# Kernel tuning notes

Hardware: AMD Instinct MI355X
Metric: run time of the kernel (lower is better)

Reference implementation:

```python
import jax, jax.numpy as jnp
import numpy as np

N4, N3, N2, N1, K = 32768, 65536, 131072, 262144, 16
G = 512


def _w(key, fan_in, fan_out):
    return jax.random.normal(key, (fan_in, fan_out), dtype=jnp.float32) / np.sqrt(fan_in)


def setup_inputs() -> dict:
    key = jax.random.key(0)
    ks = jax.random.split(key, 24)

    def edges(k, n_coarse, n_fine):
        # each fine (output) point gathers from K random coarse (input) points
        src = jax.random.randint(k, (n_fine * K,), 0, n_coarse, dtype=jnp.int32)
        dst = jnp.repeat(jnp.arange(n_fine, dtype=jnp.int32), K)
        return src, dst

    src3, dst3 = edges(ks[0], N4, N3)
    src2, dst2 = edges(ks[1], N3, N2)
    src1, dst1 = edges(ks[2], N2, N1)

    def gidx(k, n):
        return jnp.sort(jax.random.randint(k, (n,), 0, G, dtype=jnp.int32))

    inp = {
        'z_mask': jax.random.normal(ks[3], (N4, 64), dtype=jnp.float32),
        'pos4': jax.random.normal(ks[4], (N4, 3), dtype=jnp.float32),
        'pos3': jax.random.normal(ks[5], (N3, 3), dtype=jnp.float32),
        'pos2': jax.random.normal(ks[6], (N2, 3), dtype=jnp.float32),
        'pos1': jax.random.normal(ks[7], (N1, 3), dtype=jnp.float32),
        'g4': gidx(ks[8], N4), 'g3': gidx(ks[9], N3),
        'g2': gidx(ks[10], N2), 'g1': gidx(ks[11], N1),
        # PointConv MLP params: Linear(c_in+3 -> c_mid), CELU, Linear(c_mid -> c_out), max-aggregate
        'w1a': _w(ks[12], 64 + 3, 64), 'b1a': jnp.zeros((64,), jnp.float32),
        'w1b': _w(ks[13], 64, 32), 'b1b': jnp.zeros((32,), jnp.float32),
        'w2a': _w(ks[14], 32 + 3, 16), 'b2a': jnp.zeros((16,), jnp.float32),
        'w2b': _w(ks[15], 16, 16), 'b2b': jnp.zeros((16,), jnp.float32),
        'w3a': _w(ks[16], 16 + 3, 8), 'b3a': jnp.zeros((8,), jnp.float32),
        'w3b': _w(ks[17], 8, 8), 'b3b': jnp.zeros((8,), jnp.float32),
        'wlin': _w(ks[18], 8, 1), 'blin': jnp.zeros((1,), jnp.float32),
        'src3': src3, 'dst3': dst3,
        'src2': src2, 'dst2': dst2,
        'src1': src1, 'dst1': dst1,
    }
    return inp


def point_conv(x_in, pos_in, pos_out, src, dst, w_a, b_a, w_b, b_b, n_out):
    # gather: per-edge neighbor features + relative positions
    rel = pos_in[src] - pos_out[dst]                      # [E, 3]
    feat = jnp.concatenate([x_in[src], rel], axis=-1)     # [E, c_in+3]
    h = jax.nn.celu(feat @ w_a + b_a)                     # [E, c_mid]
    m = h @ w_b + b_b                                     # [E, c_out]
    # scatter: max-aggregate edge messages onto output points
    return jax.ops.segment_max(m, dst, num_segments=n_out)


def reference(z_mask, pos4, pos3, pos2, pos1, g4, g3, g2, g1,
              w1a, b1a, w1b, b1b, w2a, b2a, w2b, b2b, w3a, b3a, w3b, b3b,
              wlin, blin, src3, dst3, src2, dst2, src1, dst1):
    out = jax.nn.celu(point_conv(z_mask, pos4, pos3, src3, dst3, w1a, b1a, w1b, b1b, N3))
    out = jax.nn.celu(point_conv(out, pos3, pos2, src2, dst2, w2a, b2a, w2b, b2b, N2))
    out = jax.nn.celu(point_conv(out, pos2, pos1, src1, dst1, w3a, b3a, w3b, b3b, N1))
    logits = out @ wlin + blin                            # [N1, 1]
    return jax.nn.log_sigmoid(logits)
```

## Files before the change

kernel.cpp:

```cpp
#include <hip/hip_runtime.h>
#include <hip/hip_fp16.h>
#include <math.h>

#define N4C 32768
#define N3C 65536
#define N2C 131072
#define N1C 262144

typedef _Float16 f16x8 __attribute__((ext_vector_type(8)));
typedef float f32x4 __attribute__((ext_vector_type(4)));
typedef float f32x16 __attribute__((ext_vector_type(16)));

__device__ __forceinline__ f32x4 mfma16(f16x8 a, f16x8 b, f32x4 c) {
  return __builtin_amdgcn_mfma_f32_16x16x32_f16(a, b, c, 0, 0, 0);
}
__device__ __forceinline__ f32x16 mfma32(f16x8 a, f16x8 b, f32x16 c) {
  return __builtin_amdgcn_mfma_f32_32x32x16_f16(a, b, c, 0, 0, 0);
}

__device__ __forceinline__ float celuf(float x) {
  return fmaxf(x, 0.f) + (__expf(fminf(x, 0.f)) - 1.f);
}

__device__ __forceinline__ float logsigf(float x) {
  float e = __expf(-fabsf(x));
  return fminf(x, 0.f) - __logf(1.f + e);
}

__device__ __forceinline__ float max3f(float a, float b, float c) {
  return fmaxf(fmaxf(a, b), c);
}

__device__ __forceinline__ _Float16 exp2_16(_Float16 x) {
  __half h; __builtin_memcpy(&h, &x, 2);
  h = hexp2(h);
  _Float16 r; __builtin_memcpy(&r, &h, 2);
  return r;
}

__device__ __forceinline__ f16x8 celu8p1(f16x8 x) {
  f16x8 z = {};
  f16x8 mx = __builtin_elementwise_max(x, z);
  f16x8 mn = __builtin_elementwise_min(x, z) * (_Float16)1.44269504f;
#pragma unroll
  for (int i = 0; i < 8; ++i) mn[i] = exp2_16(mn[i]);
  return mx + mn;
}

__global__ __launch_bounds__(256) void y4_kernel(
    const float* __restrict__ z, const float* __restrict__ pos4,
    const float* __restrict__ pos3, const float* __restrict__ w1a,
    const float* __restrict__ b1a, _Float16* __restrict__ y4,
    _Float16* __restrict__ vt3) {
  if (blockIdx.x >= 512) {
    const int idx = (blockIdx.x - 512) * 256 + threadIdx.x;
    const int p = idx >> 3, seg = (idx & 7) * 8;
    const float q0 = pos3[p * 3 + 0];
    const float q1 = pos3[p * 3 + 1];
    const float q2 = pos3[p * 3 + 2];
    f16x8 v;
#pragma unroll
    for (int j = 0; j < 8; ++j) {
      const int k = seg + j;
      v[j] = (_Float16)(w1a[64 * 64 + k] * q0 + w1a[65 * 64 + k] * q1 +
                        w1a[66 * 64 + k] * q2);
    }
    *(f16x8*)(vt3 + (size_t)p * 64 + seg) = v;
    return;
  }
  const int lane = threadIdx.x & 63, wid = threadIdx.x >> 6;
  const int col = lane & 15, quad = lane >> 4;
  const int base = (blockIdx.x * 4 + wid) * 16;

  f16x8 Ba[2][4];
#pragma unroll
  for (int c = 0; c < 2; ++c)
#pragma unroll
    for (int t = 0; t < 4; ++t)
#pragma unroll
      for (int j = 0; j < 8; ++j)
        Ba[c][t][j] = (_Float16)w1a[(c * 32 + quad * 8 + j) * 64 + t * 16 + col];

  float wr[3][4];
#pragma unroll
  for (int c = 0; c < 3; ++c)
#pragma unroll
    for (int t = 0; t < 4; ++t)
      wr[c][t] = w1a[(64 + c) * 64 + t * 16 + col];

  float px[4], py[4], pz[4];
#pragma unroll
  for (int r = 0; r < 4; ++r) {
    const int row = base + quad * 4 + r;
    px[r] = pos4[row * 3 + 0];
    py[r] = pos4[row * 3 + 1];
    pz[r] = pos4[row * 3 + 2];
  }

  const float* zr = z + (size_t)(base + col) * 64;
  f16x8 A0, A1;
  {
    float4 f0 = *(const float4*)(zr + quad * 8);
    float4 f1 = *(const float4*)(zr + quad * 8 + 4);
    float4 f2 = *(const float4*)(zr + 32 + quad * 8);
    float4 f3 = *(const float4*)(zr + 32 + quad * 8 + 4);
    A0[0] = (_Float16)f0.x; A0[1] = (_Float16)f0.y; A0[2] = (_Float16)f0.z; A0[3] = (_Float16)f0.w;
    A0[4] = (_Float16)f1.x; A0[5] = (_Float16)f1.y; A0[6] = (_Float16)f1.z; A0[7] = (_Float16)f1.w;
    A1[0] = (_Float16)f2.x; A1[1] = (_Float16)f2.y; A1[2] = (_Float16)f2.z; A1[3] = (_Float16)f2.w;
    A1[4] = (_Float16)f3.x; A1[5] = (_Float16)f3.y; A1[6] = (_Float16)f3.z; A1[7] = (_Float16)f3.w;
  }
#pragma unroll
  for (int t = 0; t < 4; ++t) {
    f32x4 acc = {0.f, 0.f, 0.f, 0.f};
    acc = mfma16(A0, Ba[0][t], acc);
    acc = mfma16(A1, Ba[1][t], acc);
    const float bt = b1a[t * 16 + col];
#pragma unroll
    for (int r = 0; r < 4; ++r) {
      const float posterm =
          px[r] * wr[0][t] + py[r] * wr[1][t] + pz[r] * wr[2][t];
      y4[(size_t)(base + quad * 4 + r) * 64 + t * 16 + col] =
          (_Float16)(acc[r] + bt + posterm);
    }
  }
}

__global__ __launch_bounds__(256) void y3_kernel(
    const _Float16* __restrict__ x3f, const float* __restrict__ pos3,
    const float* __restrict__ pos2, const float* __restrict__ w2a,
    const float* __restrict__ b2a, _Float16* __restrict__ y3,
    _Float16* __restrict__ vt2) {
  if (blockIdx.x >= 1024) {
    const int idx = (blockIdx.x - 1024) * 256 + threadIdx.x;
    const int p = idx >> 1, seg = (idx & 1) * 8;
    const float q0 = pos2[p * 3 + 0];
    const float q1 = pos2[p * 3 + 1];
    const float q2 = pos2[p * 3 + 2];
    f16x8 v;
#pragma unroll
    for (int j = 0; j < 8; ++j) {
      const int k = seg + j;
      v[j] = (_Float16)(w2a[32 * 16 + k] * q0 + w2a[33 * 16 + k] * q1 +
                        w2a[34 * 16 + k] * q2);
    }
    *(f16x8*)(vt2 + (size_t)p * 16 + seg) = v;
    return;
  }
  const int lane = threadIdx.x & 63, wid = threadIdx.x >> 6;
  const int col = lane & 15, quad = lane >> 4;
  const int base = (blockIdx.x * 4 + wid) * 16;

  f16x8 B;
#pragma unroll
  for (int j = 0; j < 8; ++j) B[j] = (_Float16)w2a[(quad * 8 + j) * 16 + col];

  float wr[3];
#pragma unroll
  for (int c = 0; c < 3; ++c) wr[c] = w2a[(32 + c) * 16 + col];

  float px[4], py[4], pz[4];
#pragma unroll
  for (int r = 0; r < 4; ++r) {
    const int row = base + quad * 4 + r;
    px[r] = pos3[row * 3 + 0];
    py[r] = pos3[row * 3 + 1];
    pz[r] = pos3[row * 3 + 2];
  }

  f16x8 A = *(const f16x8*)(x3f + (size_t)(base + col) * 32 + quad * 8);
  f32x4 d = {0.f, 0.f, 0.f, 0.f};
  d = mfma16(A, B, d);
  const float bt = b2a[col];
#pragma unroll
  for (int r = 0; r < 4; ++r) {
    const float posterm = px[r] * wr[0] + py[r] * wr[1] + pz[r] * wr[2];
    y3[(size_t)(base + quad * 4 + r) * 16 + col] =
        (_Float16)(d[r] + bt + posterm);
  }
}

__global__ __launch_bounds__(256) void y2_kernel(
    const _Float16* __restrict__ x2f, const float* __restrict__ pos2,
    const float* __restrict__ pos1, const float* __restrict__ w3a,
    const float* __restrict__ b3a, _Float16* __restrict__ y2,
    _Float16* __restrict__ vt1) {
  if (blockIdx.x >= 2048) {
    const int p = (blockIdx.x - 2048) * 256 + threadIdx.x;
    const float q0 = pos1[p * 3 + 0];
    const float q1 = pos1[p * 3 + 1];
    const float q2 = pos1[p * 3 + 2];
    f16x8 v;
#pragma unroll
    for (int k = 0; k < 8; ++k)
      v[k] = (_Float16)(w3a[16 * 8 + k] * q0 + w3a[17 * 8 + k] * q1 +
                        w3a[18 * 8 + k] * q2);
    *(f16x8*)(vt1 + (size_t)p * 8) = v;
    return;
  }
  const int lane = threadIdx.x & 63, wid = threadIdx.x >> 6;
  const int col = lane & 15, quad = lane >> 4;
  const int base = (blockIdx.x * 4 + wid) * 16;

  f16x8 B;
#pragma unroll
  for (int j = 0; j < 8; ++j) {
    int k = quad * 8 + j;
    B[j] = (k < 16 && col < 8) ? (_Float16)w3a[k * 8 + col] : (_Float16)0.f;
  }
  f16x8 A = *(const f16x8*)(x2f + (size_t)(base + col) * 16 + (quad & 1) * 8);
  f32x4 d = {0.f, 0.f, 0.f, 0.f};
  d = mfma16(A, B, d);
  if (col < 8) {
    float wr[3];
#pragma unroll
    for (int c = 0; c < 3; ++c) wr[c] = w3a[(16 + c) * 8 + col];
    const float bt = b3a[col];
#pragma unroll
    for (int r = 0; r < 4; ++r) {
      const int row = base + quad * 4 + r;
      const float posterm = pos2[row * 3 + 0] * wr[0] +
                            pos2[row * 3 + 1] * wr[1] +
                            pos2[row * 3 + 2] * wr[2];
      y2[(size_t)row * 8 + col] = (_Float16)(d[r] + bt + posterm);
    }
  }
}

__global__ __launch_bounds__(256) void l3_kernel(
    const _Float16* __restrict__ y4, const _Float16* __restrict__ vt3,
    const int* __restrict__ src3, const float* __restrict__ w1b,
    const float* __restrict__ b1b, _Float16* __restrict__ x3f) {
  const int lane = threadIdx.x & 63, wid = threadIdx.x >> 6;
  const int n = lane & 31;
  const int kh = lane >> 5;

  f16x8 Bb[4];
#pragma unroll
  for (int ks = 0; ks < 4; ++ks)
#pragma unroll
    for (int j = 0; j < 8; ++j)
      Bb[ks][j] = (_Float16)w1b[(ks * 16 + kh * 8 + j) * 32 + n];

  float s = 0.f;
#pragma unroll 4
  for (int k = 0; k < 32; ++k) s += w1b[(kh * 32 + k) * 32 + n];
  s += __shfl_xor(s, 32, 64);
  const float biasB = b1b[n] - s;

  const int gwave = blockIdx.x * 4 + wid;
  const int nw = gridDim.x << 2;

#pragma unroll 1
  for (int pb = gwave * 2; pb < N3C; pb += nw * 2) {
    const int s1 = src3[pb * 16 + n];
    const int p = pb + (n >> 4);
    const _Float16* yrow = y4 + (size_t)s1 * 64 + kh * 8;
    const _Float16* vrow = vt3 + (size_t)p * 64 + kh * 8;

    f16x8 A[4];
#pragma unroll
    for (int ks = 0; ks < 4; ++ks)
      A[ks] = *(const f16x8*)(yrow + ks * 16) - *(const f16x8*)(vrow + ks * 16);
#pragma unroll
    for (int ks = 0; ks < 4; ++ks) A[ks] = celu8p1(A[ks]);

    f32x16 acc = {};
#pragma unroll
    for (int ks = 0; ks < 4; ++ks) acc = mfma32(A[ks], Bb[ks], acc);

    float mA = fmaxf(max3f(max3f(acc[0], acc[1], acc[2]),
                           max3f(acc[3], acc[4], acc[5]), acc[6]), acc[7]);
    float mB = fmaxf(max3f(max3f(acc[8], acc[9], acc[10]),
                           max3f(acc[11], acc[12], acc[13]), acc[14]), acc[15]);
    mA = fmaxf(mA, __shfl_xor(mA, 32, 64));
    mB = fmaxf(mB, __shfl_xor(mB, 32, 64));

    const float mv = kh ? mB : mA;
    x3f[(size_t)(pb + kh) * 32 + n] = (_Float16)celuf(mv + biasB);
  }
}

__device__ __forceinline__ void l2_compute(
    int pr, f16x8 A_in, f16x8 vt, f16x8 Bb, float biasB, int kh, int n,
    _Float16* __restrict__ x2f) {
  f16x8 A = celu8p1(A_in - vt);
  f32x16 acc = {};
  acc = mfma32(A, Bb, acc);

  float mA = fmaxf(max3f(max3f(acc[0], acc[1], acc[2]),
                         max3f(acc[3], acc[4], acc[5]), acc[6]), acc[7]);
  float mB = fmaxf(max3f(max3f(acc[8], acc[9], acc[10]),
                         max3f(acc[11], acc[12], acc[13]), acc[14]), acc[15]);
  mA = fmaxf(mA, __shfl_xor(mA, 32, 64));
  mB = fmaxf(mB, __shfl_xor(mB, 32, 64));

  if (n < 16) {
    const float m = kh ? mB : mA;
    x2f[(size_t)(2 * pr + kh) * 16 + n] = (_Float16)celuf(m + biasB);
  }
}

__global__ __launch_bounds__(256) void l2_kernel(
    const _Float16* __restrict__ y3, const _Float16* __restrict__ vt2,
    const int* __restrict__ src2, const float* __restrict__ w2b,
    const float* __restrict__ b2b, _Float16* __restrict__ x2f) {
  const int lane = threadIdx.x & 63, wid = threadIdx.x >> 6;
  const int n = lane & 31;
  const int e = lane & 15;
  const int h = (lane >> 4) & 1;
  const int kh = lane >> 5;

  f16x8 Bb;
#pragma unroll
  for (int j = 0; j < 8; ++j)
    Bb[j] = (n < 16) ? (_Float16)w2b[(kh * 8 + j) * 16 + n] : (_Float16)0.f;
  float ws = 0.f;
#pragma unroll
  for (int k = 0; k < 16; ++k) ws += w2b[k * 16 + (n & 15)];
  const float biasB = b2b[n & 15] - ws;

  const int gwave = blockIdx.x * 4 + wid;
  const int nw = gridDim.x << 2;

#pragma unroll 1
  for (int pr = gwave; pr < N2C / 2; pr += 2 * nw) {
    const int pr2 = pr + nw;
    const int pa = 2 * pr + h, pb = 2 * pr2 + h;
    const int sa = src2[pa * 16 + e];
    const int sb = src2[pb * 16 + e];

    f16x8 Aa = *(const f16x8*)(y3 + (size_t)sa * 16 + kh * 8);
    f16x8 Ab = *(const f16x8*)(y3 + (size_t)sb * 16 + kh * 8);
    f16x8 va = *(const f16x8*)(vt2 + (size_t)pa * 16 + kh * 8);
    f16x8 vb = *(const f16x8*)(vt2 + (size_t)pb * 16 + kh * 8);

    l2_compute(pr,  Aa, va, Bb, biasB, kh, n, x2f);
    l2_compute(pr2, Ab, vb, Bb, biasB, kh, n, x2f);
  }
}

__device__ __forceinline__ void l1_compute(
    int pb, f16x8 A_in, f16x8 vt, f16x8 Bb, float biasB, float wl, float bl,
    int lane, float* __restrict__ out) {
  f16x8 A = celu8p1(A_in - vt);
  f32x16 acc = {};
  acc = mfma32(A, Bb, acc);

  float mA = fmaxf(max3f(max3f(acc[0], acc[1], acc[2]),
                         max3f(acc[3], acc[4], acc[5]), acc[6]), acc[7]);
  float mB = fmaxf(max3f(max3f(acc[8], acc[9], acc[10]),
                         max3f(acc[11], acc[12], acc[13]), acc[14]), acc[15]);
  mA = fmaxf(mA, __shfl_xor(mA, 32, 64));
  mB = fmaxf(mB, __shfl_xor(mB, 32, 64));

  float tA = celuf(mA + biasB) * wl;
  float tB = celuf(mB + biasB) * wl;
  tA += __shfl_xor(tA, 1, 64);
  tA += __shfl_xor(tA, 2, 64);
  tA += __shfl_xor(tA, 4, 64);
  tB += __shfl_xor(tB, 1, 64);
  tB += __shfl_xor(tB, 2, 64);
  tB += __shfl_xor(tB, 4, 64);
  if (lane == 0) {
    float2 o; o.x = logsigf(tA + bl); o.y = logsigf(tB + bl);
    *(float2*)(out + pb) = o;
  } else if (lane == 8) {
    float2 o; o.x = logsigf(tA + bl); o.y = logsigf(tB + bl);
    *(float2*)(out + pb + 2) = o;
  }
}

__global__ __launch_bounds__(256) void l1_kernel(
    const _Float16* __restrict__ y2, const _Float16* __restrict__ vt1,
    const int* __restrict__ src1, const float* __restrict__ w3b,
    const float* __restrict__ b3b, const float* __restrict__ wlin,
    const float* __restrict__ blin, float* __restrict__ out) {
  const int lane = threadIdx.x & 63, wid = threadIdx.x >> 6;
  const int m = lane & 31;
  const int e = lane & 15;
  const int h = (lane >> 4) & 1;
  const int kh = lane >> 5;
  const int g = 2 * kh + h;

  f16x8 Bb;
  const int n = m;
#pragma unroll
  for (int j = 0; j < 8; ++j)
    Bb[j] = (n < 16 && (n >> 3) == kh) ? (_Float16)w3b[j * 8 + (n & 7)]
                                       : (_Float16)0.f;
  float ws = 0.f;
#pragma unroll
  for (int j = 0; j < 8; ++j) ws += w3b[j * 8 + (n & 7)];
  const float biasB = (n < 16) ? b3b[n & 7] - ws : 0.f;
  const float wl = (n < 16) ? wlin[n & 7] : 0.f;
  const float bl = blin[0];

  const int gwave = blockIdx.x * 4 + wid;
  const int nw = gridDim.x << 2;

#pragma unroll 1
  for (int q = gwave; q < N1C / 4; q += 2 * nw) {
    const int q2 = q + nw;
    const int pba = q * 4, pbb = q2 * 4;
    const int pa = pba + g, pb = pbb + g;
    const int sa = src1[pa * 16 + e];
    const int sb = src1[pb * 16 + e];

    f16x8 Aa = *(const f16x8*)(y2 + (size_t)sa * 8);
    f16x8 Ab = *(const f16x8*)(y2 + (size_t)sb * 8);
    f16x8 va = *(const f16x8*)(vt1 + (size_t)pa * 8);
    f16x8 vb = *(const f16x8*)(vt1 + (size_t)pb * 8);

    l1_compute(pba, Aa, va, Bb, biasB, wl, bl, lane, out);
    l1_compute(pbb, Ab, vb, Bb, biasB, wl, bl, lane, out);
  }
}

extern "C" void kernel_launch(void* const* d_in, const int* in_sizes, int n_in,
                              void* d_out, int out_size, void* d_ws, size_t ws_size,
                              hipStream_t stream) {
  const float* z_mask = (const float*)d_in[0];
  const float* pos4 = (const float*)d_in[1];
  const float* pos3 = (const float*)d_in[2];
  const float* pos2 = (const float*)d_in[3];
  const float* pos1 = (const float*)d_in[4];
  const float* w1a = (const float*)d_in[9];
  const float* b1a = (const float*)d_in[10];
  const float* w1b = (const float*)d_in[11];
  const float* b1b = (const float*)d_in[12];
  const float* w2a = (const float*)d_in[13];
  const float* b2a = (const float*)d_in[14];
  const float* w2b = (const float*)d_in[15];
  const float* b2b = (const float*)d_in[16];
  const float* w3a = (const float*)d_in[17];
  const float* b3a = (const float*)d_in[18];
  const float* w3b = (const float*)d_in[19];
  const float* b3b = (const float*)d_in[20];
  const float* wlin = (const float*)d_in[21];
  const float* blin = (const float*)d_in[22];
  const int* src3 = (const int*)d_in[23];
  const int* src2 = (const int*)d_in[25];
  const int* src1 = (const int*)d_in[27];

  char* w = (char*)d_ws;
  _Float16* y4  = (_Float16*)(w);
  _Float16* vt3 = (_Float16*)(w + (4u << 20));
  _Float16* x3f = (_Float16*)(w + (12u << 20));
  _Float16* y3  = (_Float16*)(w);
  _Float16* vt2 = (_Float16*)(w + (4u << 20));
  _Float16* x2f = (_Float16*)(w + (8u << 20));
  _Float16* y2  = (_Float16*)(w + (2u << 20));
  _Float16* vt1 = (_Float16*)(w + (12u << 20));
  float* out = (float*)d_out;

  y4_kernel<<<2560, 256, 0, stream>>>(z_mask, pos4, pos3, w1a, b1a, y4, vt3);
  l3_kernel<<<2048, 256, 0, stream>>>(y4, vt3, src3, w1b, b1b, x3f);
  y3_kernel<<<2048, 256, 0, stream>>>(x3f, pos3, pos2, w2a, b2a, y3, vt2);
  l2_kernel<<<2048, 256, 0, stream>>>(y3, vt2, src2, w2b, b2b, x2f);
  y2_kernel<<<3072, 256, 0, stream>>>(x2f, pos2, pos1, w3a, b3a, y2, vt1);
  l1_kernel<<<2048, 256, 0, stream>>>(y2, vt1, src1, w3b, b3b,
                                      wlin, blin, out);
}
```

Measured before the change: 235.0 us.

## Software-pipeline edge index loads and deepen per-wave work in gather kernels

The three gather kernels now prefetch the next iteration's source indices before processing the current one, so the index-load latency overlaps the dependent feature gathers and MFMA work. L2 and L1 move from two to three points per iteration, with bounds guards. L3 uses a fixed four-iteration loop with a hardcoded stride of 8192 waves, which assumes a specific grid size. These changes raise register pressure and couple L3 correctness to the launch configuration.

```diff
diff --git a/kernel.cpp b/kernel.cpp
--- a/kernel.cpp
+++ b/kernel.cpp
@@ -226,6 +226,36 @@
   }
 }
 
+__device__ __forceinline__ void l3_body(
+    int pb, int s1, int kh, int n, const _Float16* __restrict__ y4,
+    const _Float16* __restrict__ vt3, const f16x8 Bb[4], float biasB,
+    _Float16* __restrict__ x3f) {
+  const int p = pb + (n >> 4);
+  const _Float16* yrow = y4 + (size_t)s1 * 64 + kh * 8;
+  const _Float16* vrow = vt3 + (size_t)p * 64 + kh * 8;
+
+  f16x8 A[4];
+#pragma unroll
+  for (int ks = 0; ks < 4; ++ks)
+    A[ks] = *(const f16x8*)(yrow + ks * 16) - *(const f16x8*)(vrow + ks * 16);
+#pragma unroll
+  for (int ks = 0; ks < 4; ++ks) A[ks] = celu8p1(A[ks]);
+
+  f32x16 acc = {};
+#pragma unroll
+  for (int ks = 0; ks < 4; ++ks) acc = mfma32(A[ks], Bb[ks], acc);
+
+  float mA = fmaxf(max3f(max3f(acc[0], acc[1], acc[2]),
+                         max3f(acc[3], acc[4], acc[5]), acc[6]), acc[7]);
+  float mB = fmaxf(max3f(max3f(acc[8], acc[9], acc[10]),
+                         max3f(acc[11], acc[12], acc[13]), acc[14]), acc[15]);
+  mA = fmaxf(mA, __shfl_xor(mA, 32, 64));
+  mB = fmaxf(mB, __shfl_xor(mB, 32, 64));
+
+  const float mv = kh ? mB : mA;
+  x3f[(size_t)(pb + kh) * 32 + n] = (_Float16)celuf(mv + biasB);
+}
+
 __global__ __launch_bounds__(256) void l3_kernel(
     const _Float16* __restrict__ y4, const _Float16* __restrict__ vt3,
     const int* __restrict__ src3, const float* __restrict__ w1b,
@@ -247,36 +277,15 @@
   s += __shfl_xor(s, 32, 64);
   const float biasB = b1b[n] - s;
 
-  const int gwave = blockIdx.x * 4 + wid;
-  const int nw = gridDim.x << 2;
-
+  const int gw = blockIdx.x * 4 + wid;
+
+  int sCur = src3[(2 * gw) * 16 + n];
 #pragma unroll 1
-  for (int pb = gwave * 2; pb < N3C; pb += nw * 2) {
-    const int s1 = src3[pb * 16 + n];
-    const int p = pb + (n >> 4);
-    const _Float16* yrow = y4 + (size_t)s1 * 64 + kh * 8;
-    const _Float16* vrow = vt3 + (size_t)p * 64 + kh * 8;
-
-    f16x8 A[4];
-#pragma unroll
-    for (int ks = 0; ks < 4; ++ks)
-      A[ks] = *(const f16x8*)(yrow + ks * 16) - *(const f16x8*)(vrow + ks * 16);
-#pragma unroll
-    for (int ks = 0; ks < 4; ++ks) A[ks] = celu8p1(A[ks]);
-
-    f32x16 acc = {};
-#pragma unroll
-    for (int ks = 0; ks < 4; ++ks) acc = mfma32(A[ks], Bb[ks], acc);
-
-    float mA = fmaxf(max3f(max3f(acc[0], acc[1], acc[2]),
-                           max3f(acc[3], acc[4], acc[5]), acc[6]), acc[7]);
-    float mB = fmaxf(max3f(max3f(acc[8], acc[9], acc[10]),
-                           max3f(acc[11], acc[12], acc[13]), acc[14]), acc[15]);
-    mA = fmaxf(mA, __shfl_xor(mA, 32, 64));
-    mB = fmaxf(mB, __shfl_xor(mB, 32, 64));
-
-    const float mv = kh ? mB : mA;
-    x3f[(size_t)(pb + kh) * 32 + n] = (_Float16)celuf(mv + biasB);
+  for (int k = 0; k < 4; ++k) {
+    const int kn = (k < 3) ? k + 1 : 3;
+    const int sNext = src3[(2 * (gw + kn * 8192)) * 16 + n];
+    l3_body(2 * (gw + k * 8192), sCur, kh, n, y4, vt3, Bb, biasB, x3f);
+    sCur = sNext;
   }
 }
 
@@ -321,21 +330,40 @@
 
   const int gwave = blockIdx.x * 4 + wid;
   const int nw = gridDim.x << 2;
+  const int lim = N2C / 2;
+
+  int sA = src2[(2 * gwave + h) * 16 + e];
+  int sB = src2[(2 * (gwave + nw) + h) * 16 + e];
+  int sC = src2[(2 * (gwave + 2 * nw) + h) * 16 + e];
 
 #pragma unroll 1
-  for (int pr = gwave; pr < N2C / 2; pr += 2 * nw) {
-    const int pr2 = pr + nw;
-    const int pa = 2 * pr + h, pb = 2 * pr2 + h;
-    const int sa = src2[pa * 16 + e];
-    const int sb = src2[pb * 16 + e];
-
-    f16x8 Aa = *(const f16x8*)(y3 + (size_t)sa * 16 + kh * 8);
-    f16x8 Ab = *(const f16x8*)(y3 + (size_t)sb * 16 + kh * 8);
-    f16x8 va = *(const f16x8*)(vt2 + (size_t)pa * 16 + kh * 8);
-    f16x8 vb = *(const f16x8*)(vt2 + (size_t)pb * 16 + kh * 8);
-
-    l2_compute(pr,  Aa, va, Bb, biasB, kh, n, x2f);
-    l2_compute(pr2, Ab, vb, Bb, biasB, kh, n, x2f);
+  for (int base = gwave; base < lim; base += 3 * nw) {
+    const bool ok1 = base + nw < lim;
+    const bool ok2 = base + 2 * nw < lim;
+    const int pr1 = ok1 ? base + nw : base;
+    const int pr2 = ok2 ? base + 2 * nw : base;
+    const int pa0 = 2 * base + h, pa1 = 2 * pr1 + h, pa2 = 2 * pr2 + h;
+
+    f16x8 Aa = *(const f16x8*)(y3 + (size_t)sA * 16 + kh * 8);
+    f16x8 va = *(const f16x8*)(vt2 + (size_t)pa0 * 16 + kh * 8);
+    f16x8 Ab = *(const f16x8*)(y3 + (size_t)sB * 16 + kh * 8);
+    f16x8 vb = *(const f16x8*)(vt2 + (size_t)pa1 * 16 + kh * 8);
+    f16x8 Ac = *(const f16x8*)(y3 + (size_t)sC * 16 + kh * 8);
+    f16x8 vc = *(const f16x8*)(vt2 + (size_t)pa2 * 16 + kh * 8);
+
+    const int nb = base + 3 * nw;
+    const int n0 = nb < lim ? nb : base;
+    const int n1 = nb + nw < lim ? nb + nw : n0;
+    const int n2 = nb + 2 * nw < lim ? nb + 2 * nw : n0;
+    const int sAn = src2[(2 * n0 + h) * 16 + e];
+    const int sBn = src2[(2 * n1 + h) * 16 + e];
+    const int sCn = src2[(2 * n2 + h) * 16 + e];
+
+    l2_compute(base, Aa, va, Bb, biasB, kh, n, x2f);
+    if (ok1) l2_compute(base + nw, Ab, vb, Bb, biasB, kh, n, x2f);
+    if (ok2) l2_compute(base + 2 * nw, Ac, vc, Bb, biasB, kh, n, x2f);
+
+    sA = sAn; sB = sBn; sC = sCn;
   }
 }
 
@@ -377,10 +405,8 @@
     const float* __restrict__ blin, float* __restrict__ out) {
   const int lane = threadIdx.x & 63, wid = threadIdx.x >> 6;
   const int m = lane & 31;
-  const int e = lane & 15;
-  const int h = (lane >> 4) & 1;
   const int kh = lane >> 5;
-  const int g = 2 * kh + h;
+  const int g = 2 * kh + ((lane >> 4) & 1);
 
   f16x8 Bb;
   const int n = m;
@@ -397,22 +423,40 @@
 
   const int gwave = blockIdx.x * 4 + wid;
   const int nw = gridDim.x << 2;
+  const int lim = N1C / 4;
+
+  int sA = src1[gwave * 64 + lane];
+  int sB = src1[(gwave + nw) * 64 + lane];
+  int sC = src1[(gwave + 2 * nw) * 64 + lane];
 
 #pragma unroll 1
-  for (int q = gwave; q < N1C / 4; q += 2 * nw) {
-    const int q2 = q + nw;
-    const int pba = q * 4, pbb = q2 * 4;
-    const int pa = pba + g, pb = pbb + g;
-    const int sa = src1[pa * 16 + e];
-    const int sb = src1[pb * 16 + e];
-
-    f16x8 Aa = *(const f16x8*)(y2 + (size_t)sa * 8);
-    f16x8 Ab = *(const f16x8*)(y2 + (size_t)sb * 8);
-    f16x8 va = *(const f16x8*)(vt1 + (size_t)pa * 8);
-    f16x8 vb = *(const f16x8*)(vt1 + (size_t)pb * 8);
-
-    l1_compute(pba, Aa, va, Bb, biasB, wl, bl, lane, out);
-    l1_compute(pbb, Ab, vb, Bb, biasB, wl, bl, lane, out);
+  for (int base = gwave; base < lim; base += 3 * nw) {
+    const bool ok1 = base + nw < lim;
+    const bool ok2 = base + 2 * nw < lim;
+    const int q1 = ok1 ? base + nw : base;
+    const int q2 = ok2 ? base + 2 * nw : base;
+    const int p0 = base * 4 + g, p1 = q1 * 4 + g, p2 = q2 * 4 + g;
+
+    f16x8 Aa = *(const f16x8*)(y2 + (size_t)sA * 8);
+    f16x8 va = *(const f16x8*)(vt1 + (size_t)p0 * 8);
+    f16x8 Ab = *(const f16x8*)(y2 + (size_t)sB * 8);
+    f16x8 vb = *(const f16x8*)(vt1 + (size_t)p1 * 8);
+    f16x8 Ac = *(const f16x8*)(y2 + (size_t)sC * 8);
+    f16x8 vc = *(const f16x8*)(vt1 + (size_t)p2 * 8);
+
+    const int nb = base + 3 * nw;
+    const int m0 = nb < lim ? nb : base;
+    const int m1 = nb + nw < lim ? nb + nw : m0;
+    const int m2 = nb + 2 * nw < lim ? nb + 2 * nw : m0;
+    const int sAn = src1[m0 * 64 + lane];
+    const int sBn = src1[m1 * 64 + lane];
+    const int sCn = src1[m2 * 64 + lane];
+
+    l1_compute(base * 4, Aa, va, Bb, biasB, wl, bl, lane, out);
+    if (ok1) l1_compute((base + nw) * 4, Ab, vb, Bb, biasB, wl, bl, lane, out);
+    if (ok2) l1_compute((base + 2 * nw) * 4, Ac, vc, Bb, biasB, wl, bl, lane, out);
+
+    sA = sAn; sB = sBn; sC = sCn;
   }
 }
 
```

Result: slower. 242.1 us (+3.0%).

## Fuse five stage kernels into one cooperative persistent kernel with grid syncs

Applied to the files above, without the earlier changes.

Replaces the five separate launches after y4 with a single cooperative kernel of 1024 blocks that runs l3, y3, l2, y2 and l1 in sequence, separated by grid.sync(). If the cooperative launch fails it falls back to the separate kernels. The aim is to remove per-launch gaps and tail effects between small, dependent kernels. The cost is fewer blocks per stage, less latency hiding in the gather-heavy stages, and grid-barrier overhead. The l1 source-index load is also rewritten as one contiguous q*64+lane read.

```diff
diff --git a/kernel.cpp b/kernel.cpp
--- a/kernel.cpp
+++ b/kernel.cpp
@@ -1,6 +1,9 @@
 #include <hip/hip_runtime.h>
 #include <hip/hip_fp16.h>
+#include <hip/hip_cooperative_groups.h>
 #include <math.h>
+
+namespace cg = cooperative_groups;
 
 #define N4C 32768
 #define N3C 65536
@@ -125,6 +128,61 @@
   }
 }
 
+
+__global__ __launch_bounds__(256) void l3_kernel(
+    const _Float16* __restrict__ y4, const _Float16* __restrict__ vt3,
+    const int* __restrict__ src3, const float* __restrict__ w1b,
+    const float* __restrict__ b1b, _Float16* __restrict__ x3f) {
+  const int lane = threadIdx.x & 63, wid = threadIdx.x >> 6;
+  const int n = lane & 31;
+  const int kh = lane >> 5;
+
+  f16x8 Bb[4];
+#pragma unroll
+  for (int ks = 0; ks < 4; ++ks)
+#pragma unroll
+    for (int j = 0; j < 8; ++j)
+      Bb[ks][j] = (_Float16)w1b[(ks * 16 + kh * 8 + j) * 32 + n];
+
+  float s = 0.f;
+#pragma unroll 4
+  for (int k = 0; k < 32; ++k) s += w1b[(kh * 32 + k) * 32 + n];
+  s += __shfl_xor(s, 32, 64);
+  const float biasB = b1b[n] - s;
+
+  const int gwave = blockIdx.x * 4 + wid;
+  const int nw = gridDim.x << 2;
+
+#pragma unroll 1
+  for (int pb = gwave * 2; pb < N3C; pb += nw * 2) {
+    const int s1 = src3[pb * 16 + n];
+    const int p = pb + (n >> 4);
+    const _Float16* yrow = y4 + (size_t)s1 * 64 + kh * 8;
+    const _Float16* vrow = vt3 + (size_t)p * 64 + kh * 8;
+
+    f16x8 A[4];
+#pragma unroll
+    for (int ks = 0; ks < 4; ++ks)
+      A[ks] = *(const f16x8*)(yrow + ks * 16) - *(const f16x8*)(vrow + ks * 16);
+#pragma unroll
+    for (int ks = 0; ks < 4; ++ks) A[ks] = celu8p1(A[ks]);
+
+    f32x16 acc = {};
+#pragma unroll
+    for (int ks = 0; ks < 4; ++ks) acc = mfma32(A[ks], Bb[ks], acc);
+
+    float mA = fmaxf(max3f(max3f(acc[0], acc[1], acc[2]),
+                           max3f(acc[3], acc[4], acc[5]), acc[6]), acc[7]);
+    float mB = fmaxf(max3f(max3f(acc[8], acc[9], acc[10]),
+                           max3f(acc[11], acc[12], acc[13]), acc[14]), acc[15]);
+    mA = fmaxf(mA, __shfl_xor(mA, 32, 64));
+    mB = fmaxf(mB, __shfl_xor(mB, 32, 64));
+
+    const float mv = kh ? mB : mA;
+    x3f[(size_t)(pb + kh) * 32 + n] = (_Float16)celuf(mv + biasB);
+  }
+}
+
 __global__ __launch_bounds__(256) void y3_kernel(
     const _Float16* __restrict__ x3f, const float* __restrict__ pos3,
     const float* __restrict__ pos2, const float* __restrict__ w2a,
@@ -223,60 +281,6 @@
                             pos2[row * 3 + 2] * wr[2];
       y2[(size_t)row * 8 + col] = (_Float16)(d[r] + bt + posterm);
     }
-  }
-}
-
-__global__ __launch_bounds__(256) void l3_kernel(
-    const _Float16* __restrict__ y4, const _Float16* __restrict__ vt3,
-    const int* __restrict__ src3, const float* __restrict__ w1b,
-    const float* __restrict__ b1b, _Float16* __restrict__ x3f) {
-  const int lane = threadIdx.x & 63, wid = threadIdx.x >> 6;
-  const int n = lane & 31;
-  const int kh = lane >> 5;
-
-  f16x8 Bb[4];
-#pragma unroll
-  for (int ks = 0; ks < 4; ++ks)
-#pragma unroll
-    for (int j = 0; j < 8; ++j)
-      Bb[ks][j] = (_Float16)w1b[(ks * 16 + kh * 8 + j) * 32 + n];
-
-  float s = 0.f;
-#pragma unroll 4
-  for (int k = 0; k < 32; ++k) s += w1b[(kh * 32 + k) * 32 + n];
-  s += __shfl_xor(s, 32, 64);
-  const float biasB = b1b[n] - s;
-
-  const int gwave = blockIdx.x * 4 + wid;
-  const int nw = gridDim.x << 2;
-
-#pragma unroll 1
-  for (int pb = gwave * 2; pb < N3C; pb += nw * 2) {
-    const int s1 = src3[pb * 16 + n];
-    const int p = pb + (n >> 4);
-    const _Float16* yrow = y4 + (size_t)s1 * 64 + kh * 8;
-    const _Float16* vrow = vt3 + (size_t)p * 64 + kh * 8;
-
-    f16x8 A[4];
-#pragma unroll
-    for (int ks = 0; ks < 4; ++ks)
-      A[ks] = *(const f16x8*)(yrow + ks * 16) - *(const f16x8*)(vrow + ks * 16);
-#pragma unroll
-    for (int ks = 0; ks < 4; ++ks) A[ks] = celu8p1(A[ks]);
-
-    f32x16 acc = {};
-#pragma unroll
-    for (int ks = 0; ks < 4; ++ks) acc = mfma32(A[ks], Bb[ks], acc);
-
-    float mA = fmaxf(max3f(max3f(acc[0], acc[1], acc[2]),
-                           max3f(acc[3], acc[4], acc[5]), acc[6]), acc[7]);
-    float mB = fmaxf(max3f(max3f(acc[8], acc[9], acc[10]),
-                           max3f(acc[11], acc[12], acc[13]), acc[14]), acc[15]);
-    mA = fmaxf(mA, __shfl_xor(mA, 32, 64));
-    mB = fmaxf(mB, __shfl_xor(mB, 32, 64));
-
-    const float mv = kh ? mB : mA;
-    x3f[(size_t)(pb + kh) * 32 + n] = (_Float16)celuf(mv + biasB);
   }
 }
 
@@ -377,10 +381,8 @@
     const float* __restrict__ blin, float* __restrict__ out) {
   const int lane = threadIdx.x & 63, wid = threadIdx.x >> 6;
   const int m = lane & 31;
-  const int e = lane & 15;
-  const int h = (lane >> 4) & 1;
   const int kh = lane >> 5;
-  const int g = 2 * kh + h;
+  const int g = 2 * kh + ((lane >> 4) & 1);
 
   f16x8 Bb;
   const int n = m;
@@ -403,8 +405,8 @@
     const int q2 = q + nw;
     const int pba = q * 4, pbb = q2 * 4;
     const int pa = pba + g, pb = pbb + g;
-    const int sa = src1[pa * 16 + e];
-    const int sb = src1[pb * 16 + e];
+    const int sa = src1[q * 64 + lane];
+    const int sb = src1[q2 * 64 + lane];
 
     f16x8 Aa = *(const f16x8*)(y2 + (size_t)sa * 8);
     f16x8 Ab = *(const f16x8*)(y2 + (size_t)sb * 8);
@@ -413,6 +415,237 @@
 
     l1_compute(pba, Aa, va, Bb, biasB, wl, bl, lane, out);
     l1_compute(pbb, Ab, vb, Bb, biasB, wl, bl, lane, out);
+  }
+}
+
+struct FArgs {
+  const _Float16* y4; const _Float16* vt3; const int* src3;
+  const float* w1b; const float* b1b; _Float16* x3f;
+  const float* pos3; const float* pos2; const float* w2a; const float* b2a;
+  _Float16* y3; _Float16* vt2;
+  const int* src2; const float* w2b; const float* b2b; _Float16* x2f;
+  const float* pos1; const float* w3a; const float* b3a;
+  _Float16* y2; _Float16* vt1;
+  const int* src1; const float* w3b; const float* b3b;
+  const float* wlin; const float* blin; float* out;
+};
+
+__global__ __launch_bounds__(256, 4) void fused_kernel(FArgs a) {
+  const cg::grid_group grid = cg::this_grid();
+  const int lane = threadIdx.x & 63, wid = threadIdx.x >> 6;
+  const int blk = blockIdx.x;
+  const int gwave = blk * 4 + wid;
+  const int nw = gridDim.x << 2;
+
+  {
+    const int n = lane & 31;
+    const int kh = lane >> 5;
+
+    f16x8 Bb[4];
+#pragma unroll
+    for (int ks = 0; ks < 4; ++ks)
+#pragma unroll
+      for (int j = 0; j < 8; ++j)
+        Bb[ks][j] = (_Float16)a.w1b[(ks * 16 + kh * 8 + j) * 32 + n];
+
+    float s = 0.f;
+#pragma unroll 4
+    for (int k = 0; k < 32; ++k) s += a.w1b[(kh * 32 + k) * 32 + n];
+    s += __shfl_xor(s, 32, 64);
+    const float biasB = a.b1b[n] - s;
+
+#pragma unroll 1
+    for (int pb = gwave * 2; pb < N3C; pb += nw * 2) {
+      const int s1 = a.src3[pb * 16 + n];
+      const int p = pb + (n >> 4);
+      const _Float16* yrow = a.y4 + (size_t)s1 * 64 + kh * 8;
+      const _Float16* vrow = a.vt3 + (size_t)p * 64 + kh * 8;
+
+      f16x8 A[4];
+#pragma unroll
+      for (int ks = 0; ks < 4; ++ks)
+        A[ks] = *(const f16x8*)(yrow + ks * 16) - *(const f16x8*)(vrow + ks * 16);
+#pragma unroll
+      for (int ks = 0; ks < 4; ++ks) A[ks] = celu8p1(A[ks]);
+
+      f32x16 acc = {};
+#pragma unroll
+      for (int ks = 0; ks < 4; ++ks) acc = mfma32(A[ks], Bb[ks], acc);
+
+      float mA = fmaxf(max3f(max3f(acc[0], acc[1], acc[2]),
+                             max3f(acc[3], acc[4], acc[5]), acc[6]), acc[7]);
+      float mB = fmaxf(max3f(max3f(acc[8], acc[9], acc[10]),
+                             max3f(acc[11], acc[12], acc[13]), acc[14]), acc[15]);
+      mA = fmaxf(mA, __shfl_xor(mA, 32, 64));
+      mB = fmaxf(mB, __shfl_xor(mB, 32, 64));
+
+      const float mv = kh ? mB : mA;
+      a.x3f[(size_t)(pb + kh) * 32 + n] = (_Float16)celuf(mv + biasB);
+    }
+  }
+  grid.sync();
+
+  {
+    const int col = lane & 15, quad = lane >> 4;
+    const int base = gwave * 16;
+
+    f16x8 B;
+#pragma unroll
+    for (int j = 0; j < 8; ++j)
+      B[j] = (_Float16)a.w2a[(quad * 8 + j) * 16 + col];
+
+    float wr[3];
+#pragma unroll
+    for (int c = 0; c < 3; ++c) wr[c] = a.w2a[(32 + c) * 16 + col];
+
+    float px[4], py[4], pz[4];
+#pragma unroll
+    for (int r = 0; r < 4; ++r) {
+      const int row = base + quad * 4 + r;
+      px[r] = a.pos3[row * 3 + 0];
+      py[r] = a.pos3[row * 3 + 1];
+      pz[r] = a.pos3[row * 3 + 2];
+    }
+
+    f16x8 A = *(const f16x8*)(a.x3f + (size_t)(base + col) * 32 + quad * 8);
+    f32x4 d = {0.f, 0.f, 0.f, 0.f};
+    d = mfma16(A, B, d);
+    const float bt = a.b2a[col];
+#pragma unroll
+    for (int r = 0; r < 4; ++r) {
+      const float posterm = px[r] * wr[0] + py[r] * wr[1] + pz[r] * wr[2];
+      a.y3[(size_t)(base + quad * 4 + r) * 16 + col] =
+          (_Float16)(d[r] + bt + posterm);
+    }
+
+    const int idx = blk * 256 + threadIdx.x;
+    const int p = idx >> 1, seg = (idx & 1) * 8;
+    const float q0 = a.pos2[p * 3 + 0];
+    const float q1 = a.pos2[p * 3 + 1];
+    const float q2 = a.pos2[p * 3 + 2];
+    f16x8 v;
+#pragma unroll
+    for (int j = 0; j < 8; ++j) {
+      const int k = seg + j;
+      v[j] = (_Float16)(a.w2a[32 * 16 + k] * q0 + a.w2a[33 * 16 + k] * q1 +
+                        a.w2a[34 * 16 + k] * q2);
+    }
+    *(f16x8*)(a.vt2 + (size_t)p * 16 + seg) = v;
+  }
+  grid.sync();
+
+  {
+    const int n = lane & 31;
+    const int e = lane & 15;
+    const int h = (lane >> 4) & 1;
+    const int kh = lane >> 5;
+
+    f16x8 Bb;
+#pragma unroll
+    for (int j = 0; j < 8; ++j)
+      Bb[j] = (n < 16) ? (_Float16)a.w2b[(kh * 8 + j) * 16 + n] : (_Float16)0.f;
+    float ws = 0.f;
+#pragma unroll
+    for (int k = 0; k < 16; ++k) ws += a.w2b[k * 16 + (n & 15)];
+    const float biasB = a.b2b[n & 15] - ws;
+
+#pragma unroll 1
+    for (int pr = gwave; pr < N2C / 2; pr += 2 * nw) {
+      const int pr2 = pr + nw;
+      const int pa = 2 * pr + h, pb = 2 * pr2 + h;
+      const int sa = a.src2[pa * 16 + e];
+      const int sb = a.src2[pb * 16 + e];
+
+      f16x8 Aa = *(const f16x8*)(a.y3 + (size_t)sa * 16 + kh * 8);
+      f16x8 Ab = *(const f16x8*)(a.y3 + (size_t)sb * 16 + kh * 8);
+      f16x8 va = *(const f16x8*)(a.vt2 + (size_t)pa * 16 + kh * 8);
+      f16x8 vb = *(const f16x8*)(a.vt2 + (size_t)pb * 16 + kh * 8);
+
+      l2_compute(pr,  Aa, va, Bb, biasB, kh, n, a.x2f);
+      l2_compute(pr2, Ab, vb, Bb, biasB, kh, n, a.x2f);
+    }
+  }
+  grid.sync();
+
+  {
+    const int col = lane & 15, quad = lane >> 4;
+#pragma unroll 1
+    for (int b2 = blk; b2 < 2048; b2 += 1024) {
+      const int base = (b2 * 4 + wid) * 16;
+
+      f16x8 B;
+#pragma unroll
+      for (int j = 0; j < 8; ++j) {
+        int k = quad * 8 + j;
+        B[j] = (k < 16 && col < 8) ? (_Float16)a.w3a[k * 8 + col]
+                                   : (_Float16)0.f;
+      }
+      f16x8 A =
+          *(const f16x8*)(a.x2f + (size_t)(base + col) * 16 + (quad & 1) * 8);
+      f32x4 d = {0.f, 0.f, 0.f, 0.f};
+      d = mfma16(A, B, d);
+      if (col < 8) {
+        float wr[3];
+#pragma unroll
+        for (int c = 0; c < 3; ++c) wr[c] = a.w3a[(16 + c) * 8 + col];
+        const float bt = a.b3a[col];
+#pragma unroll
+        for (int r = 0; r < 4; ++r) {
+          const int row = base + quad * 4 + r;
+          const float posterm = a.pos2[row * 3 + 0] * wr[0] +
+                                a.pos2[row * 3 + 1] * wr[1] +
+                                a.pos2[row * 3 + 2] * wr[2];
+          a.y2[(size_t)row * 8 + col] = (_Float16)(d[r] + bt + posterm);
+        }
+      }
+    }
+    const int p = blk * 256 + threadIdx.x;
+    const float q0 = a.pos1[p * 3 + 0];
+    const float q1 = a.pos1[p * 3 + 1];
+    const float q2 = a.pos1[p * 3 + 2];
+    f16x8 v;
+#pragma unroll
+    for (int k = 0; k < 8; ++k)
+      v[k] = (_Float16)(a.w3a[16 * 8 + k] * q0 + a.w3a[17 * 8 + k] * q1 +
+                        a.w3a[18 * 8 + k] * q2);
+    *(f16x8*)(a.vt1 + (size_t)p * 8) = v;
+  }
+  grid.sync();
+
+  {
+    const int m = lane & 31;
+    const int kh = lane >> 5;
+    const int g = 2 * kh + ((lane >> 4) & 1);
+
+    f16x8 Bb;
+    const int n = m;
+#pragma unroll
+    for (int j = 0; j < 8; ++j)
+      Bb[j] = (n < 16 && (n >> 3) == kh) ? (_Float16)a.w3b[j * 8 + (n & 7)]
+                                         : (_Float16)0.f;
+    float ws = 0.f;
+#pragma unroll
+    for (int j = 0; j < 8; ++j) ws += a.w3b[j * 8 + (n & 7)];
+    const float biasB = (n < 16) ? a.b3b[n & 7] - ws : 0.f;
+    const float wl = (n < 16) ? a.wlin[n & 7] : 0.f;
+    const float bl = a.blin[0];
+
+#pragma unroll 1
+    for (int q = gwave; q < N1C / 4; q += 2 * nw) {
+      const int q2 = q + nw;
+      const int pba = q * 4, pbb = q2 * 4;
+      const int pa = pba + g, pb = pbb + g;
+      const int sa = a.src1[q * 64 + lane];
+      const int sb = a.src1[q2 * 64 + lane];
+
+      f16x8 Aa = *(const f16x8*)(a.y2 + (size_t)sa * 8);
+      f16x8 Ab = *(const f16x8*)(a.y2 + (size_t)sb * 8);
+      f16x8 va = *(const f16x8*)(a.vt1 + (size_t)pa * 8);
+      f16x8 vb = *(const f16x8*)(a.vt1 + (size_t)pb * 8);
+
+      l1_compute(pba, Aa, va, Bb, biasB, wl, bl, lane, a.out);
+      l1_compute(pbb, Ab, vb, Bb, biasB, wl, bl, lane, a.out);
+    }
   }
 }
 
@@ -454,10 +687,29 @@
   float* out = (float*)d_out;
 
   y4_kernel<<<2560, 256, 0, stream>>>(z_mask, pos4, pos3, w1a, b1a, y4, vt3);
-  l3_kernel<<<2048, 256, 0, stream>>>(y4, vt3, src3, w1b, b1b, x3f);
-  y3_kernel<<<2048, 256, 0, stream>>>(x3f, pos3, pos2, w2a, b2a, y3, vt2);
-  l2_kernel<<<2048, 256, 0, stream>>>(y3, vt2, src2, w2b, b2b, x2f);
-  y2_kernel<<<3072, 256, 0, stream>>>(x2f, pos2, pos1, w3a, b3a, y2, vt1);
-  l1_kernel<<<2048, 256, 0, stream>>>(y2, vt1, src1, w3b, b3b,
-                                      wlin, blin, out);
-}
+
+  FArgs fa;
+  fa.y4 = y4; fa.vt3 = vt3; fa.src3 = src3;
+  fa.w1b = w1b; fa.b1b = b1b; fa.x3f = x3f;
+  fa.pos3 = pos3; fa.pos2 = pos2; fa.w2a = w2a; fa.b2a = b2a;
+  fa.y3 = y3; fa.vt2 = vt2;
+  fa.src2 = src2; fa.w2b = w2b; fa.b2b = b2b; fa.x2f = x2f;
+  fa.pos1 = pos1; fa.w3a = w3a; fa.b3a = b3a;
+  fa.y2 = y2; fa.vt1 = vt1;
+  fa.src1 = src1; fa.w3b = w3b; fa.b3b = b3b;
+  fa.wlin = wlin; fa.blin = blin; fa.out = out;
+
+  void* args[] = {&fa};
+  hipError_t err = hipLaunchCooperativeKernel(
+      (const void*)fused_kernel, dim3(1024), dim3(256), args, 0, stream);
+
+  if (err != hipSuccess) {
+    (void)hipGetLastError();
+    l3_kernel<<<2048, 256, 0, stream>>>(y4, vt3, src3, w1b, b1b, x3f);
+    y3_kernel<<<2048, 256, 0, stream>>>(x3f, pos3, pos2, w2a, b2a, y3, vt2);
+    l2_kernel<<<2048, 256, 0, stream>>>(y3, vt2, src2, w2b, b2b, x2f);
+    y2_kernel<<<3072, 256, 0, stream>>>(x2f, pos2, pos1, w3a, b3a, y2, vt1);
+    l1_kernel<<<2048, 256, 0, stream>>>(y2, vt1, src1, w3b, b3b,
+                                        wlin, blin, out);
+  }
+}
```

After: 754.7 us. 3.21x slower.
